# Kernel tuning notes

Measured on AMD Instinct MI355X. Metric: run time of the kernel, lower is better.

The kernel has to match this reference:

```python
import jax, jax.numpy as jnp
import numpy as np

NUM_OBJ_CLS = 151


def setup_inputs() -> dict:
    key = jax.random.key(0)
    ks = jax.random.split(key, 12)
    N, H, E, U, P, R = 6144, 512, 49152, 2048, 4096, 51
    return {
        "edge_ctx": jax.random.normal(ks[0], (N, H), jnp.float32),
        "union_features": jax.random.normal(ks[1], (E, U), jnp.float32),
        "W_post_emb": jax.random.normal(ks[2], (H, 2 * H), jnp.float32) * (H ** -0.5),
        "b_post_emb": jnp.zeros((2 * H,), jnp.float32),
        "W_post_cat": jax.random.normal(ks[3], (2 * H, P), jnp.float32) * ((2 * H) ** -0.5),
        "b_post_cat": jnp.zeros((P,), jnp.float32),
        "W_up": jax.random.normal(ks[4], (U, P), jnp.float32) * (U ** -0.5),
        "b_up": jnp.zeros((P,), jnp.float32),
        "W_rel": jax.random.normal(ks[5], (P, R), jnp.float32) * (P ** -0.5),
        "b_rel": jnp.zeros((R,), jnp.float32),
        "freq_table": jax.random.normal(ks[6], (NUM_OBJ_CLS * NUM_OBJ_CLS, R), jnp.float32),
        "obj_preds": jax.random.randint(ks[7], (N,), 0, NUM_OBJ_CLS, jnp.int64),
        "pair_idx": jax.random.randint(ks[8], (E, 2), 0, N, jnp.int64),
    }


def reference(edge_ctx, union_features, W_post_emb, b_post_emb, W_post_cat,
              b_post_cat, W_up, b_up, W_rel, b_rel, freq_table,
              obj_preds, pair_idx):
    N, H = edge_ctx.shape
    # post_emb -> split into head/tail representations [N, H] each
    edge_rep = (edge_ctx @ W_post_emb + b_post_emb).reshape(N, 2, H)
    head_rep, tail_rep = edge_rep[:, 0], edge_rep[:, 1]
    # gather per-pair head/tail reps and concat -> [E, 2H]
    prod_rep = jnp.concatenate(
        (head_rep[pair_idx[:, 0]], tail_rep[pair_idx[:, 1]]), axis=-1)
    prod_rep = prod_rep @ W_post_cat + b_post_cat            # [E, P]
    # union feature up-projection (union_single_not_match) and gating multiply
    prod_rep = prod_rep * (union_features @ W_up + b_up)     # [E, P]
    rel_dists = prod_rep @ W_rel + b_rel                     # [E, R]
    # frequency-bias lookup indexed by (head_class, tail_class)
    bias_idx = obj_preds[pair_idx[:, 0]] * NUM_OBJ_CLS + obj_preds[pair_idx[:, 1]]
    rel_dists = rel_dists + freq_table[bias_idx]
    return rel_dists
```

## Files before the change

### kernel.cpp

```cpp
#include <hip/hip_runtime.h>

typedef unsigned short u16;
typedef __attribute__((ext_vector_type(4))) float f32x4;
typedef __attribute__((ext_vector_type(4))) u16 u16x4;
typedef __attribute__((ext_vector_type(8))) u16 u16x8;
typedef __attribute__((ext_vector_type(8))) short short8;

__device__ __forceinline__ u16 f2bf(float f) {
  unsigned int u = __builtin_bit_cast(unsigned int, f);
  u += 0x7FFFu + ((u >> 16) & 1u);
  return (u16)(u >> 16);
}
__device__ __forceinline__ float bf2f(u16 b) {
  unsigned int u = ((unsigned int)b) << 16;
  return __builtin_bit_cast(float, u);
}

__device__ __forceinline__ void gld16(const void* g, void* l) {
  __builtin_amdgcn_global_load_lds(
      (const __attribute__((address_space(1))) unsigned int*)g,
      (__attribute__((address_space(3))) unsigned int*)l, 16, 0, 0);
}

template <int N>
__device__ __forceinline__ void boundary() {
  asm volatile("s_waitcnt vmcnt(%0)" ::"n"(N) : "memory");
  __builtin_amdgcn_s_barrier();
  asm volatile("" ::: "memory");
  __builtin_amdgcn_sched_barrier(0);
}


__global__ __launch_bounds__(256) void cvt_f32_bf16(const float* __restrict__ s,
                                                    u16* __restrict__ d, long n4) {
  long stride = (long)gridDim.x * 256;
  for (long i = (long)blockIdx.x * 256 + threadIdx.x; i < n4; i += stride) {
    f32x4 v = *(const f32x4*)(s + i * 4);
    u16x4 o = {f2bf(v.x), f2bf(v.y), f2bf(v.z), f2bf(v.w)};
    *(u16x4*)(d + i * 4) = o;
  }
}

__global__ __launch_bounds__(256) void transpose_f32_bf16(const float* __restrict__ src,
                                                          u16* __restrict__ dst,
                                                          int R, int C, int CP) {
  __shared__ float tile[32][33];
  int r0 = blockIdx.x * 32, c0 = blockIdx.y * 32;
  int tx = threadIdx.x & 31, ty = threadIdx.x >> 5;
#pragma unroll
  for (int i = 0; i < 32; i += 8) {
    int r = r0 + ty + i, c = c0 + tx;
    tile[ty + i][tx] = (r < R && c < C) ? src[(size_t)r * C + c] : 0.f;
  }
  __syncthreads();
#pragma unroll
  for (int i = 0; i < 32; i += 8) {
    int c = c0 + ty + i, r = r0 + tx;
    if (c < CP && r < R) dst[(size_t)c * R + r] = f2bf(tile[tx][ty + i]);
  }
}


template <int NROW>
__device__ __forceinline__ void stage_direct(const u16* __restrict__ src, int ld,
                                             int kcol0, u16* lds, int tid) {
#pragma unroll
  for (int it = 0; it < NROW / 32; ++it) {
    int idx = it * 256 + tid;
    int row = idx >> 3, c = idx & 7;
    int cc = c ^ (row & 7);
    gld16(src + (size_t)row * ld + kcol0 + cc * 8, (char*)lds + idx * 16);
  }
}

template <int MI>
__device__ __forceinline__ void mma_step(const char* As, const char* Bs, int arow0,
                                         int brow0, int lane, f32x4 acc[MI][4]) {
  int r = lane & 15, q = lane >> 4;
#pragma unroll
  for (int ks = 0; ks < 2; ++ks) {
    short8 a[MI], b[4];
#pragma unroll
    for (int i = 0; i < MI; ++i) {
      int row = arow0 + i * 16 + r;
      a[i] = *(const short8*)(As + row * 128 + ((((ks << 2) + q) ^ (row & 7)) << 4));
    }
#pragma unroll
    for (int j = 0; j < 4; ++j) {
      int row = brow0 + j * 16 + r;
      b[j] = *(const short8*)(Bs + row * 128 + ((((ks << 2) + q) ^ (row & 7)) << 4));
    }
#pragma unroll
    for (int i = 0; i < MI; ++i)
#pragma unroll
      for (int j = 0; j < 4; ++j)
        acc[i][j] = __builtin_amdgcn_mfma_f32_16x16x32_bf16(a[i], b[j], acc[i][j], 0, 0, 0);
  }
}


__global__ __launch_bounds__(256) void gemm1(const u16* __restrict__ ec,
                                             const u16* __restrict__ WpeT,
                                             const float* __restrict__ bpe,
                                             u16* __restrict__ head,
                                             u16* __restrict__ tail) {
  __shared__ __align__(16) u16 As[128 * 64];
  __shared__ __align__(16) u16 Bs[128 * 64];
  int tid = threadIdx.x, lane = tid & 63, wave = tid >> 6;
  int wrow = wave >> 1, wcol = wave & 1;
  int m0 = blockIdx.x * 128, n0 = blockIdx.y * 128;
  f32x4 z = {0.f, 0.f, 0.f, 0.f};
  f32x4 acc[4][4];
#pragma unroll
  for (int i = 0; i < 4; ++i)
#pragma unroll
    for (int j = 0; j < 4; ++j) acc[i][j] = z;

  for (int kb = 0; kb < 8; ++kb) {
    stage_direct<128>(ec + (size_t)m0 * 512, 512, kb * 64, As, tid);
    stage_direct<128>(WpeT + (size_t)n0 * 512, 512, kb * 64, Bs, tid);
    __syncthreads();
    mma_step<4>((const char*)As, (const char*)Bs, wrow * 64, wcol * 64, lane, acc);
    __syncthreads();
  }
  int r = lane & 15, q = lane >> 4;
#pragma unroll
  for (int i = 0; i < 4; ++i) {
    int e = m0 + wrow * 64 + i * 16 + q * 4;
#pragma unroll
    for (int j = 0; j < 4; ++j) {
      int c = n0 + wcol * 64 + j * 16 + r;
      float bb = bpe[c];
#pragma unroll
      for (int g = 0; g < 4; ++g) {
        float v = acc[i][j][g] + bb;
        if (c < 512) head[(size_t)(e + g) * 512 + c] = f2bf(v);
        else         tail[(size_t)(e + g) * 512 + (c - 512)] = f2bf(v);
      }
    }
  }
}


__global__ __launch_bounds__(256) void gemm_hp(const u16* __restrict__ A,
                                               const u16* __restrict__ BT,
                                               u16* __restrict__ P) {
  __shared__ __align__(16) u16 As[128 * 64];
  __shared__ __align__(16) u16 Bs[128 * 64];
  int tid = threadIdx.x, lane = tid & 63, wave = tid >> 6;
  int wrow = wave >> 1, wcol = wave & 1;
  int m0 = blockIdx.x * 128, n0 = blockIdx.y * 128;
  f32x4 z = {0.f, 0.f, 0.f, 0.f};
  f32x4 acc[4][4];
#pragma unroll
  for (int i = 0; i < 4; ++i)
#pragma unroll
    for (int j = 0; j < 4; ++j) acc[i][j] = z;

  for (int kb = 0; kb < 8; ++kb) {
    stage_direct<128>(A + (size_t)m0 * 512, 512, kb * 64, As, tid);
    stage_direct<128>(BT + (size_t)n0 * 512, 512, kb * 64, Bs, tid);
    __syncthreads();
    mma_step<4>((const char*)As, (const char*)Bs, wrow * 64, wcol * 64, lane, acc);
    __syncthreads();
  }
  int r = lane & 15, q = lane >> 4;
#pragma unroll
  for (int i = 0; i < 4; ++i) {
    int e = m0 + wrow * 64 + i * 16 + q * 4;
#pragma unroll
    for (int j = 0; j < 4; ++j) {
      int c = n0 + wcol * 64 + j * 16 + r;
#pragma unroll
      for (int g = 0; g < 4; ++g)
        P[(size_t)(e + g) * 4096 + c] = f2bf(acc[i][j][g]);
    }
  }
}


__global__ __launch_bounds__(512, 2) void gemm_union_8ph(
    const u16* __restrict__ U, const u16* __restrict__ WupT,
    const float* __restrict__ bup, const float* __restrict__ bpc,
    const u16* __restrict__ Hp, const u16* __restrict__ Tp,
    const int* __restrict__ pair, u16* __restrict__ T) {
  extern __shared__ __align__(16) u16 lds[];
  const int tid = threadIdx.x, lane = tid & 63, wave = tid >> 6;
  const int wm = wave >> 2, wn = wave & 3;
  const int r = lane & 15, q = lane >> 4;

  int bid = blockIdx.x;
  int swz = (bid & 7) * 384 + (bid >> 3);
  int m0 = (swz >> 4) * 256, n0 = (swz & 15) * 256;

  const u16* Apanel = U + (size_t)m0 * 2048;
  const u16* Bpanel = WupT + (size_t)n0 * 2048;

  f32x4 acc[8][4];
  f32x4 z = {0.f, 0.f, 0.f, 0.f};
#pragma unroll
  for (int i = 0; i < 8; ++i)
#pragma unroll
    for (int j = 0; j < 4; ++j) acc[i][j] = z;

  auto STAGE = [&](int buf, int mat, int kt, int kh) {
    const u16* src = mat ? Bpanel : Apanel;
#pragma unroll
    for (int it = 0; it < 2; ++it) {
      int id = it * 512 + tid;
      int row = id >> 2, c4 = id & 3;
      gld16(src + (size_t)row * 2048 + kt * 64 + kh * 32 + ((c4 ^ ((row >> 1) & 3)) << 3),
            lds + ((((buf << 1) | mat) << 1 | kh) << 13) + id * 8);
    }
  };
  auto LDA = [&](int buf, int kh, int mi) -> short8 {
    int row = wm * 128 + mi * 16 + r;
    return *(const short8*)(lds + (((buf << 1) << 1 | kh) << 13) + row * 32 +
                            ((q ^ ((r >> 1) & 3)) << 3));
  };
  auto LDB = [&](int buf, int kh, int nj) -> short8 {
    int row = wn * 64 + nj * 16 + r;
    return *(const short8*)(lds + ((((buf << 1) | 1) << 1 | kh) << 13) + row * 32 +
                            ((q ^ ((r >> 1) & 3)) << 3));
  };

  STAGE(0, 0, 0, 0);
  STAGE(0, 1, 0, 0);
  STAGE(0, 0, 0, 1);
  STAGE(0, 1, 0, 1);
  boundary<4>();

  short8 a[4], b[4];
  const int NT = 32;
  for (int t = 0; t < NT; ++t) {
    int cur = t & 1, nxt = cur ^ 1;
    bool more = (t < NT - 1);

#pragma unroll
    for (int nj = 0; nj < 4; ++nj) b[nj] = LDB(cur, 0, nj);
#pragma unroll
    for (int mi = 0; mi < 4; ++mi) a[mi] = LDA(cur, 0, mi);
    if (more) STAGE(nxt, 0, t + 1, 0);
    __builtin_amdgcn_s_setprio(1);
#pragma unroll
    for (int mi = 0; mi < 4; ++mi)
#pragma unroll
      for (int nj = 0; nj < 4; ++nj)
        acc[mi][nj] = __builtin_amdgcn_mfma_f32_16x16x32_bf16(a[mi], b[nj], acc[mi][nj], 0, 0, 0);
    __builtin_amdgcn_s_setprio(0);

#pragma unroll
    for (int mi = 0; mi < 4; ++mi) a[mi] = LDA(cur, 0, mi + 4);
    if (more) STAGE(nxt, 1, t + 1, 0);
    __builtin_amdgcn_s_setprio(1);
#pragma unroll
    for (int mi = 0; mi < 4; ++mi)
#pragma unroll
      for (int nj = 0; nj < 4; ++nj)
        acc[mi + 4][nj] = __builtin_amdgcn_mfma_f32_16x16x32_bf16(a[mi], b[nj], acc[mi + 4][nj], 0, 0, 0);
    __builtin_amdgcn_s_setprio(0);

    if (t == NT - 1) boundary<0>(); else boundary<4>();

#pragma unroll
    for (int nj = 0; nj < 4; ++nj) b[nj] = LDB(cur, 1, nj);
#pragma unroll
    for (int mi = 0; mi < 4; ++mi) a[mi] = LDA(cur, 1, mi);
    if (more) STAGE(nxt, 0, t + 1, 1);
    __builtin_amdgcn_s_setprio(1);
#pragma unroll
    for (int mi = 0; mi < 4; ++mi)
#pragma unroll
      for (int nj = 0; nj < 4; ++nj)
        acc[mi][nj] = __builtin_amdgcn_mfma_f32_16x16x32_bf16(a[mi], b[nj], acc[mi][nj], 0, 0, 0);
    __builtin_amdgcn_s_setprio(0);

#pragma unroll
    for (int mi = 0; mi < 4; ++mi) a[mi] = LDA(cur, 1, mi + 4);
    if (more) STAGE(nxt, 1, t + 1, 1);
    __builtin_amdgcn_s_setprio(1);
#pragma unroll
    for (int mi = 0; mi < 4; ++mi)
#pragma unroll
      for (int nj = 0; nj < 4; ++nj)
        acc[mi + 4][nj] = __builtin_amdgcn_mfma_f32_16x16x32_bf16(a[mi], b[nj], acc[mi + 4][nj], 0, 0, 0);
    __builtin_amdgcn_s_setprio(0);

    if (more) boundary<4>();
  }

  __syncthreads();

  u16* Uw = lds + (wave << 13);
#pragma unroll
  for (int mi = 0; mi < 8; ++mi) {
#pragma unroll
    for (int nj = 0; nj < 4; ++nj) {
      int col = nj * 16 + r;
      float bb = bup[n0 + wn * 64 + col];
#pragma unroll
      for (int g = 0; g < 4; ++g) {
        int rw = mi * 16 + q * 4 + g;
        int byte_off = rw * 128 + ((((col >> 3) ^ (rw & 7)) << 4)) + (col & 7) * 2;
        *(u16*)((char*)Uw + byte_off) = f2bf(acc[mi][nj][g] + bb);
      }
    }
  }
  asm volatile("s_waitcnt lgkmcnt(0)" ::: "memory");
  __builtin_amdgcn_sched_barrier(0);

  int c0 = n0 + wn * 64;
#pragma unroll
  for (int rr = 0; rr < 2; ++rr) {
    int lr = lane * 2 + rr;
    int e = m0 + wm * 128 + lr;
    int h = pair[2 * e], tt = pair[2 * e + 1];
    const u16* hp = Hp + (size_t)h * 4096 + c0;
    const u16* tp = Tp + (size_t)tt * 4096 + c0;
    u16* dst = T + (size_t)e * 4096 + c0;
#pragma unroll
    for (int ch = 0; ch < 8; ++ch) {
      u16x8 hv = *(const u16x8*)(hp + ch * 8);
      u16x8 tv = *(const u16x8*)(tp + ch * 8);
      u16x8 uv = *(const u16x8*)((char*)Uw + lr * 128 + ((ch ^ (lr & 7)) << 4));
      u16x8 o;
#pragma unroll
      for (int k = 0; k < 8; ++k) {
        float p = bf2f(hv[k]) + bf2f(tv[k]) + bpc[c0 + ch * 8 + k];
        o[k] = f2bf(bf2f(uv[k]) * p);
      }
      *(u16x8*)(dst + ch * 8) = o;
    }
  }
}


__global__ __launch_bounds__(256) void gemm4(const u16* __restrict__ T,
                                             const u16* __restrict__ WrelT,
                                             const float* __restrict__ brel,
                                             const float* __restrict__ freq,
                                             const int* __restrict__ obj,
                                             const int* __restrict__ pair,
                                             float* __restrict__ out) {
  __shared__ __align__(16) u16 As[128 * 64];
  __shared__ __align__(16) u16 Bs[64 * 64];
  int tid = threadIdx.x, lane = tid & 63, wave = tid >> 6;
  int m0 = blockIdx.x * 128;
  f32x4 z = {0.f, 0.f, 0.f, 0.f};
  f32x4 acc[2][4];
#pragma unroll
  for (int i = 0; i < 2; ++i)
#pragma unroll
    for (int j = 0; j < 4; ++j) acc[i][j] = z;

  for (int kb = 0; kb < 64; ++kb) {
    stage_direct<128>(T + (size_t)m0 * 4096, 4096, kb * 64, As, tid);
    stage_direct<64>(WrelT, 4096, kb * 64, Bs, tid);
    __syncthreads();
    mma_step<2>((const char*)As, (const char*)Bs, wave * 32, 0, lane, acc);
    __syncthreads();
  }
  int r = lane & 15, q = lane >> 4;
#pragma unroll
  for (int i = 0; i < 2; ++i) {
    int e0r = m0 + wave * 32 + i * 16 + q * 4;
#pragma unroll
    for (int j = 0; j < 4; ++j) {
      int c = j * 16 + r;
      if (c < 51) {
        float bb = brel[c];
#pragma unroll
        for (int g = 0; g < 4; ++g) {
          int e = e0r + g;
          int bidx = obj[pair[2 * e]] * 151 + obj[pair[2 * e + 1]];
          out[(size_t)e * 51 + c] = acc[i][j][g] + bb + freq[(size_t)bidx * 51 + c];
        }
      }
    }
  }
}


extern "C" void kernel_launch(void* const* d_in, const int* in_sizes, int n_in,
                              void* d_out, int out_size, void* d_ws, size_t ws_size,
                              hipStream_t stream) {
  const float* edge_ctx = (const float*)d_in[0];
  const float* unionf   = (const float*)d_in[1];
  const float* Wpe      = (const float*)d_in[2];
  const float* bpe      = (const float*)d_in[3];
  const float* Wpc      = (const float*)d_in[4];
  const float* bpc      = (const float*)d_in[5];
  const float* Wup      = (const float*)d_in[6];
  const float* bup      = (const float*)d_in[7];
  const float* Wrel     = (const float*)d_in[8];
  const float* brel     = (const float*)d_in[9];
  const float* freq     = (const float*)d_in[10];
  const int*   obj      = (const int*)d_in[11];
  const int*   pair     = (const int*)d_in[12];
  float* out = (float*)d_out;

  u16* ws = (u16*)d_ws;
  u16* Tb      = ws;
  u16* ub      = ws + 201326592;
  u16* ec      = ws + 301989888;
  u16* head    = ws + 305135616;
  u16* tail    = ws + 308281344;
  u16* WpeT    = ws + 311427072;
  u16* WpcTopT = ws + 311951360;
  u16* WpcBotT = ws + 314048512;
  u16* WupT    = ws + 316145664;
  u16* WrelT   = ws + 324534272;
  u16* Hp      = ws + 324796416;
  u16* Tp      = ws + 349962240;

  cvt_f32_bf16<<<768, 256, 0, stream>>>(edge_ctx, ec, 786432);
  cvt_f32_bf16<<<4096, 256, 0, stream>>>(unionf, ub, 25165824);
  transpose_f32_bf16<<<dim3(16, 32), 256, 0, stream>>>(Wpe, WpeT, 512, 1024, 1024);
  transpose_f32_bf16<<<dim3(16, 128), 256, 0, stream>>>(Wpc, WpcTopT, 512, 4096, 4096);
  transpose_f32_bf16<<<dim3(16, 128), 256, 0, stream>>>(Wpc + (size_t)512 * 4096, WpcBotT, 512, 4096, 4096);
  transpose_f32_bf16<<<dim3(64, 128), 256, 0, stream>>>(Wup, WupT, 2048, 4096, 4096);
  transpose_f32_bf16<<<dim3(128, 2), 256, 0, stream>>>(Wrel, WrelT, 4096, 51, 64);

  gemm1<<<dim3(48, 8), 256, 0, stream>>>(ec, WpeT, bpe, head, tail);
  gemm_hp<<<dim3(48, 32), 256, 0, stream>>>(head, WpcTopT, Hp);
  gemm_hp<<<dim3(48, 32), 256, 0, stream>>>(tail, WpcBotT, Tp);
  gemm_union_8ph<<<3072, 512, 131072, stream>>>(ub, WupT, bup, bpc, Hp, Tp, pair, Tb);
  gemm4<<<dim3(384), 256, 0, stream>>>(Tb, WrelT, brel, freq, obj, pair, out);
}
```

Before: 1.446 ms.

## Fuse final Wrel projection into union GEMM epilogue with split-K partial reduction

New measurement: 1.298 ms. -10.3%, faster.

```diff
diff --git a/kernel.cpp b/kernel.cpp
--- a/kernel.cpp
+++ b/kernel.cpp
@@ -179,11 +179,12 @@
 }
 
 
-__global__ __launch_bounds__(512, 2) void gemm_union_8ph(
+__global__ __launch_bounds__(512, 2) void gemm_union_fuse4(
     const u16* __restrict__ U, const u16* __restrict__ WupT,
     const float* __restrict__ bup, const float* __restrict__ bpc,
     const u16* __restrict__ Hp, const u16* __restrict__ Tp,
-    const int* __restrict__ pair, u16* __restrict__ T) {
+    const int* __restrict__ pair, const u16* __restrict__ WrelT,
+    float* __restrict__ Pp) {
   extern __shared__ __align__(16) u16 lds[];
   const int tid = threadIdx.x, lane = tid & 63, wave = tid >> 6;
   const int wm = wave >> 2, wn = wave & 3;
@@ -317,66 +318,84 @@
     int h = pair[2 * e], tt = pair[2 * e + 1];
     const u16* hp = Hp + (size_t)h * 4096 + c0;
     const u16* tp = Tp + (size_t)tt * 4096 + c0;
-    u16* dst = T + (size_t)e * 4096 + c0;
 #pragma unroll
     for (int ch = 0; ch < 8; ++ch) {
       u16x8 hv = *(const u16x8*)(hp + ch * 8);
       u16x8 tv = *(const u16x8*)(tp + ch * 8);
-      u16x8 uv = *(const u16x8*)((char*)Uw + lr * 128 + ((ch ^ (lr & 7)) << 4));
+      u16* slot = (u16*)((char*)Uw + lr * 128 + ((ch ^ (lr & 7)) << 4));
+      u16x8 uv = *(u16x8*)slot;
       u16x8 o;
 #pragma unroll
       for (int k = 0; k < 8; ++k) {
         float p = bf2f(hv[k]) + bf2f(tv[k]) + bpc[c0 + ch * 8 + k];
         o[k] = f2bf(bf2f(uv[k]) * p);
       }
-      *(u16x8*)(dst + ch * 8) = o;
-    }
-  }
-}
-
-
-__global__ __launch_bounds__(256) void gemm4(const u16* __restrict__ T,
-                                             const u16* __restrict__ WrelT,
-                                             const float* __restrict__ brel,
-                                             const float* __restrict__ freq,
-                                             const int* __restrict__ obj,
-                                             const int* __restrict__ pair,
-                                             float* __restrict__ out) {
-  __shared__ __align__(16) u16 As[128 * 64];
-  __shared__ __align__(16) u16 Bs[64 * 64];
-  int tid = threadIdx.x, lane = tid & 63, wave = tid >> 6;
-  int m0 = blockIdx.x * 128;
-  f32x4 z = {0.f, 0.f, 0.f, 0.f};
-  f32x4 acc[2][4];
+      *(u16x8*)slot = o;
+    }
+  }
+  __syncthreads();
+
+  f32x4 acc2[2][4];
 #pragma unroll
   for (int i = 0; i < 2; ++i)
 #pragma unroll
-    for (int j = 0; j < 4; ++j) acc[i][j] = z;
-
-  for (int kb = 0; kb < 64; ++kb) {
-    stage_direct<128>(T + (size_t)m0 * 4096, 4096, kb * 64, As, tid);
-    stage_direct<64>(WrelT, 4096, kb * 64, Bs, tid);
-    __syncthreads();
-    mma_step<2>((const char*)As, (const char*)Bs, wave * 32, 0, lane, acc);
-    __syncthreads();
-  }
-  int r = lane & 15, q = lane >> 4;
+    for (int j = 0; j < 4; ++j) acc2[i][j] = z;
+
+#pragma unroll
+  for (int ks = 0; ks < 8; ++ks) {
+    int wn_k = ks >> 1;
+    int cb = (ks & 1) * 4;
+    short8 a2[2], b2[4];
+#pragma unroll
+    for (int i = 0; i < 2; ++i) {
+      int rr2 = wave * 32 + i * 16 + r;
+      int reg = ((rr2 >> 7) << 2) | wn_k;
+      int lr2 = rr2 & 127;
+      int ch = cb + q;
+      a2[i] = *(const short8*)((char*)lds + reg * 16384 + lr2 * 128 +
+                               ((ch ^ (lr2 & 7)) << 4));
+    }
+#pragma unroll
+    for (int j = 0; j < 4; ++j)
+      b2[j] = *(const short8*)(WrelT + (size_t)(j * 16 + r) * 4096 + n0 + ks * 32 + q * 8);
+#pragma unroll
+    for (int i = 0; i < 2; ++i)
+#pragma unroll
+      for (int j = 0; j < 4; ++j)
+        acc2[i][j] = __builtin_amdgcn_mfma_f32_16x16x32_bf16(a2[i], b2[j], acc2[i][j], 0, 0, 0);
+  }
+
+  int nt = n0 >> 8;
 #pragma unroll
   for (int i = 0; i < 2; ++i) {
-    int e0r = m0 + wave * 32 + i * 16 + q * 4;
 #pragma unroll
     for (int j = 0; j < 4; ++j) {
-      int c = j * 16 + r;
-      if (c < 51) {
-        float bb = brel[c];
-#pragma unroll
-        for (int g = 0; g < 4; ++g) {
-          int e = e0r + g;
-          int bidx = obj[pair[2 * e]] * 151 + obj[pair[2 * e + 1]];
-          out[(size_t)e * 51 + c] = acc[i][j][g] + bb + freq[(size_t)bidx * 51 + c];
-        }
+      int col = j * 16 + r;
+#pragma unroll
+      for (int g = 0; g < 4; ++g) {
+        int e = m0 + wave * 32 + i * 16 + q * 4 + g;
+        Pp[((size_t)nt * 49152 + e) * 64 + col] = acc2[i][j][g];
       }
     }
+  }
+}
+
+
+__global__ __launch_bounds__(256) void reduce_out(const float* __restrict__ Pp,
+                                                  const float* __restrict__ brel,
+                                                  const float* __restrict__ freq,
+                                                  const int* __restrict__ obj,
+                                                  const int* __restrict__ pair,
+                                                  float* __restrict__ out) {
+  int e = blockIdx.x * 4 + (threadIdx.x >> 6);
+  int c = threadIdx.x & 63;
+  const float* p = Pp + (size_t)e * 64 + c;
+  float s = 0.f;
+#pragma unroll
+  for (int nt = 0; nt < 16; ++nt) s += p[(size_t)nt * 49152 * 64];
+  if (c < 51) {
+    int bidx = obj[pair[2 * e]] * 151 + obj[pair[2 * e + 1]];
+    out[(size_t)e * 51 + c] = s + brel[c] + freq[(size_t)bidx * 51 + c];
   }
 }
 
@@ -400,7 +419,7 @@
   float* out = (float*)d_out;
 
   u16* ws = (u16*)d_ws;
-  u16* Tb      = ws;
+  float* Pp    = (float*)ws;
   u16* ub      = ws + 201326592;
   u16* ec      = ws + 301989888;
   u16* head    = ws + 305135616;
@@ -424,6 +443,6 @@
   gemm1<<<dim3(48, 8), 256, 0, stream>>>(ec, WpeT, bpe, head, tail);
   gemm_hp<<<dim3(48, 32), 256, 0, stream>>>(head, WpcTopT, Hp);
   gemm_hp<<<dim3(48, 32), 256, 0, stream>>>(tail, WpcBotT, Tp);
-  gemm_union_8ph<<<3072, 512, 131072, stream>>>(ub, WupT, bup, bpc, Hp, Tp, pair, Tb);
-  gemm4<<<dim3(384), 256, 0, stream>>>(Tb, WrelT, brel, freq, obj, pair, out);
-}
+  gemm_union_fuse4<<<3072, 512, 131072, stream>>>(ub, WupT, bup, bpc, Hp, Tp, pair, WrelT, Pp);
+  reduce_out<<<12288, 256, 0, stream>>>(Pp, brel, freq, obj, pair, out);
+}
```
